# Performance work log

Measured on AMD Instinct MI355X. Metric: run time of the kernel, lower is better.

## Reference

```python
import jax, jax.numpy as jnp
import numpy as np

B, N, C, Q, H, RATIO = 8, 8700, 256, 300, 8, 4
D = C // H
HID = C * RATIO
EPS = 1e-5


def _ln(x, w, b):
    m = jnp.mean(x, axis=-1, keepdims=True)
    v = jnp.mean((x - m) ** 2, axis=-1, keepdims=True)
    return (x - m) * jax.lax.rsqrt(v + EPS) * w + b


def setup_inputs() -> dict:
    key = jax.random.key(0)
    ks = jax.random.split(key, 8)
    s = 0.02
    return {
        "x": jax.random.normal(ks[0], (B, N, C), jnp.float32),
        # linear weights stored [in, out] (y = x @ W), no biases (qkv_bias=False, Mlp bias=False)
        "Wq": jax.random.normal(ks[1], (C, C), jnp.float32) * s,
        "Wk": jax.random.normal(ks[2], (C, C), jnp.float32) * s,
        "Wv": jax.random.normal(ks[3], (C, C), jnp.float32) * s,
        "Wp": jax.random.normal(ks[4], (C, C), jnp.float32) * s,
        "W1": jax.random.normal(ks[5], (C, HID), jnp.float32) * s,
        "W2": jax.random.normal(ks[6], (HID, C), jnp.float32) * s,
        "ln1_w": jnp.ones((C,), jnp.float32),
        "ln1_b": jnp.zeros((C,), jnp.float32),
        "ln2_w": jnp.ones((C,), jnp.float32),
        "ln2_b": jnp.zeros((C,), jnp.float32),
        "gamma1": jnp.ones((C,), jnp.float32),
        "gamma2": jnp.ones((C,), jnp.float32),
    }


def reference(x, Wq, Wk, Wv, Wp, W1, W2, ln1_w, ln1_b, ln2_w, ln2_b, gamma1, gamma2):
    scale = D ** -0.5
    xn = _ln(x, ln1_w, ln1_b)                       # [B,N,C]
    # SAQAttn: queries only from the first Q tokens; keys/values from all N tokens
    q = (xn[:, :Q] @ Wq).reshape(B, Q, H, D) * scale  # [B,Q,H,D]
    k = (xn @ Wk).reshape(B, N, H, D)
    v = (xn @ Wv).reshape(B, N, H, D)
    attn = jax.nn.softmax(jnp.einsum('bqhd,bnhd->bhqn', q, k), axis=-1)  # [B,H,Q,N]
    x_det = jnp.einsum('bhqn,bnhd->bqhd', attn, v).reshape(B, Q, C) @ Wp  # [B,Q,C]
    # residual with layer-scale gamma1; context tokens pass normed features through
    x_attn = jnp.concatenate([x_det, xn[:, Q:]], axis=1)
    x = x + gamma1 * x_attn
    # tokens_norm=False: norm2 only on query tokens
    x = jnp.concatenate([_ln(x[:, :Q], ln2_w, ln2_b), x[:, Q:]], axis=1)
    # MLP on query tokens with layer-scale gamma2 (exact GELU, as nn.GELU default)
    det = gamma2 * (jax.nn.gelu(x[:, :Q] @ W1, approximate=False) @ W2)
    # faithful to source: x_res + cat([det, x[:,Q:]]) doubles the context tokens
    return x + jnp.concatenate([det, x[:, Q:]], axis=1)
```

## Files before the change

kernel.cpp:

```cpp
#include <hip/hip_runtime.h>

#define BB 8
#define NN 8700
#define CC 256
#define QQ 300
#define HH 8
#define DD 32
#define HIDN 1024
#define NSPLIT 12
#define TSTR (NSPLIT * 64)

typedef unsigned short u16;
typedef __attribute__((ext_vector_type(8))) short short8;
typedef __attribute__((ext_vector_type(4))) float f32x4;

#define MFMA16(a, b, c) __builtin_amdgcn_mfma_f32_16x16x32_bf16((a), (b), (c), 0, 0, 0)

__device__ __forceinline__ u16 f2bu(float f) {
    unsigned int u = __builtin_bit_cast(unsigned int, f);
    u += 0x7fffu + ((u >> 16) & 1u);
    return (u16)(u >> 16);
}
__device__ __forceinline__ unsigned int cvtpk(float lo, float hi) {
    unsigned int r;
    asm("v_cvt_pk_bf16_f32 %0, %1, %2" : "=v"(r) : "v"(lo), "v"(hi));
    return r;
}

__global__ __launch_bounds__(256)
void wprep_all(const float* __restrict__ Wq, const float* __restrict__ Wk,
               const float* __restrict__ Wv, const float* __restrict__ Wp,
               const float* __restrict__ W1, const float* __restrict__ W2,
               u16* __restrict__ dst, float qscale)
{
    int e = blockIdx.x * 256 + threadIdx.x;
    float v;
    if (e < 65536)       { int i = e;          int n = i >> 8, k = i & 255;   v = Wq[k * 256 + n] * qscale; }
    else if (e < 131072) { int i = e - 65536;  int n = i >> 8, k = i & 255;   v = Wk[k * 256 + n]; }
    else if (e < 196608) { int i = e - 131072; int n = i >> 8, k = i & 255;   v = Wv[k * 256 + n]; }
    else if (e < 262144) { int i = e - 196608; int n = i >> 8, k = i & 255;   v = Wp[k * 256 + n]; }
    else if (e < 524288) { int i = e - 262144; int n = i >> 8, k = i & 255;   v = W1[k * 1024 + n]; }
    else                 { int i = e - 524288; int n = i >> 10, k = i & 1023; v = W2[k * 256 + n]; }
    dst[e] = f2bu(v);
}

__global__ __launch_bounds__(256)
void ln1_k(const float* __restrict__ x, const float* __restrict__ w,
           const float* __restrict__ bv, const float* __restrict__ g1,
           u16* __restrict__ xn, float* __restrict__ out)
{
    int row = blockIdx.x * 4 + (threadIdx.x >> 6);
    int l = threadIdx.x & 63;
    size_t base = (size_t)row * CC + l * 4;
    float4 xv = *reinterpret_cast<const float4*>(x + base);
    float s  = xv.x + xv.y + xv.z + xv.w;
    float s2 = xv.x * xv.x + xv.y * xv.y + xv.z * xv.z + xv.w * xv.w;
#pragma unroll
    for (int m = 1; m < 64; m <<= 1) {
        s  += __shfl_xor(s,  m, 64);
        s2 += __shfl_xor(s2, m, 64);
    }
    float mean = s * (1.0f / CC);
    float rs = rsqrtf(s2 * (1.0f / CC) - mean * mean + 1e-5f);
    float4 wv = *reinterpret_cast<const float4*>(w  + l * 4);
    float4 bb = *reinterpret_cast<const float4*>(bv + l * 4);
    float n0 = (xv.x - mean) * rs * wv.x + bb.x;
    float n1 = (xv.y - mean) * rs * wv.y + bb.y;
    float n2 = (xv.z - mean) * rs * wv.z + bb.z;
    float n3 = (xv.w - mean) * rs * wv.w + bb.w;
    ushort4 u; u.x = f2bu(n0); u.y = f2bu(n1); u.z = f2bu(n2); u.w = f2bu(n3);
    *reinterpret_cast<ushort4*>(xn + base) = u;
    int n = row % NN;
    if (n >= QQ) {
        float4 gv = *reinterpret_cast<const float4*>(g1 + l * 4);
        float4 o;
        o.x = 2.0f * (xv.x + gv.x * n0);
        o.y = 2.0f * (xv.y + gv.y * n1);
        o.z = 2.0f * (xv.z + gv.z * n2);
        o.w = 2.0f * (xv.w + gv.w * n3);
        *reinterpret_cast<float4*>(out + base) = o;
    }
}

__global__ __launch_bounds__(256)
void ln2_k(const float* __restrict__ x, const float* __restrict__ pd,
           const float* __restrict__ g1, const float* __restrict__ w,
           const float* __restrict__ bv, float* __restrict__ xqf, u16* __restrict__ xqb)
{
    int r = blockIdx.x * 4 + (threadIdx.x >> 6);
    int l = threadIdx.x & 63;
    int b = r / QQ, n = r - b * QQ;
    size_t xoff = ((size_t)b * NN + n) * CC + l * 4;
    size_t roff = (size_t)r * CC + l * 4;
    float4 xv = *reinterpret_cast<const float4*>(x + xoff);
    float4 pv = *reinterpret_cast<const float4*>(pd + roff);
    float4 gv = *reinterpret_cast<const float4*>(g1 + l * 4);
    float x0 = xv.x + gv.x * pv.x;
    float x1 = xv.y + gv.y * pv.y;
    float x2 = xv.z + gv.z * pv.z;
    float x3 = xv.w + gv.w * pv.w;
    float s  = x0 + x1 + x2 + x3;
    float s2 = x0 * x0 + x1 * x1 + x2 * x2 + x3 * x3;
#pragma unroll
    for (int m = 1; m < 64; m <<= 1) {
        s  += __shfl_xor(s,  m, 64);
        s2 += __shfl_xor(s2, m, 64);
    }
    float mean = s * (1.0f / CC);
    float rs = rsqrtf(s2 * (1.0f / CC) - mean * mean + 1e-5f);
    float4 wv = *reinterpret_cast<const float4*>(w  + l * 4);
    float4 bb = *reinterpret_cast<const float4*>(bv + l * 4);
    float n0 = (x0 - mean) * rs * wv.x + bb.x;
    float n1 = (x1 - mean) * rs * wv.y + bb.y;
    float n2 = (x2 - mean) * rs * wv.z + bb.z;
    float n3 = (x3 - mean) * rs * wv.w + bb.w;
    float4 o; o.x = n0; o.y = n1; o.z = n2; o.w = n3;
    *reinterpret_cast<float4*>(xqf + roff) = o;
    ushort4 u; u.x = f2bu(n0); u.y = f2bu(n1); u.z = f2bu(n2); u.w = f2bu(n3);
    *reinterpret_cast<ushort4*>(xqb + roff) = u;
}

template<int EPI>
__global__ __launch_bounds__(256)
void gemm_k(const u16* __restrict__ A, const u16* __restrict__ WT,
            u16* __restrict__ Cb, u16* __restrict__ Cb2, float* __restrict__ Cf,
            const float* __restrict__ basep, const float* __restrict__ gvec,
            float* __restrict__ outp,
            int M, int K, int ldC, int rpb, int bstr)
{
    const int w = threadIdx.x >> 6, l = threadIdx.x & 63;
    const int l15 = l & 15, kg = l >> 4;
    const int rowbase = blockIdx.x * 64;
    const int colbase = blockIdx.y * 256 + w * 64;
    const short8 z8 = {0, 0, 0, 0, 0, 0, 0, 0};
    const f32x4 fz = {0.f, 0.f, 0.f, 0.f};

    const u16* ap[4]; bool av[4];
#pragma unroll
    for (int mi = 0; mi < 4; mi++) {
        int r = rowbase + mi * 16 + l15;
        av[mi] = (r < M);
        int rr = av[mi] ? r : 0;
        size_t ar = (size_t)(rr / rpb) * bstr + (rr % rpb);
        ap[mi] = A + ar * K + kg * 8;
    }
    const u16* bp[4];
#pragma unroll
    for (int ni = 0; ni < 4; ni++) {
        int col = colbase + ni * 16 + l15;
        bp[ni] = WT + (size_t)col * K + kg * 8;
    }
    f32x4 acc[4][4];
#pragma unroll
    for (int mi = 0; mi < 4; mi++)
#pragma unroll
        for (int ni = 0; ni < 4; ni++) acc[mi][ni] = fz;

    for (int ks = 0; ks < K; ks += 32) {
        short8 a[4], bfr[4];
#pragma unroll
        for (int mi = 0; mi < 4; mi++)
            a[mi] = av[mi] ? *reinterpret_cast<const short8*>(ap[mi] + ks) : z8;
#pragma unroll
        for (int ni = 0; ni < 4; ni++)
            bfr[ni] = *reinterpret_cast<const short8*>(bp[ni] + ks);
#pragma unroll
        for (int mi = 0; mi < 4; mi++)
#pragma unroll
            for (int ni = 0; ni < 4; ni++)
                acc[mi][ni] = MFMA16(a[mi], bfr[ni], acc[mi][ni]);
    }
#pragma unroll
    for (int mi = 0; mi < 4; mi++) {
#pragma unroll
        for (int j = 0; j < 4; j++) {
            int r = rowbase + mi * 16 + kg * 4 + j;
            if (r >= M) continue;
#pragma unroll
            for (int ni = 0; ni < 4; ni++) {
                int col = colbase + ni * 16 + l15;
                float v = acc[mi][ni][j];
                if (EPI == 0) {
                    if (col < CC) Cb[(size_t)r * ldC + col] = f2bu(v);
                    else          Cb2[(size_t)r * ldC + (col - CC)] = f2bu(v);
                } else if (EPI == 1) {
                    float gl = 0.5f * v * (1.0f + erff(v * 0.70710678118654752f));
                    Cb[(size_t)r * ldC + col] = f2bu(gl);
                } else if (EPI == 2) {
                    Cf[(size_t)r * ldC + col] = v;
                } else {
                    float res = basep[(size_t)r * CC + col] + gvec[col] * v;
                    size_t orow = (size_t)(r / QQ) * NN + (r % QQ);
                    outp[orow * CC + col] = res;
                }
            }
        }
    }
}

__global__ __launch_bounds__(256)
void attn_k(const u16* __restrict__ qm, const u16* __restrict__ km,
            const u16* __restrict__ vm, float* __restrict__ Op,
            float* __restrict__ lp)
{
    __shared__ u16 vt[2][32 * 64];
    __shared__ u16 plds[4][2][16 * 64];

    const int bx = blockIdx.x;
    const int split = bx >> 6;
    const int rem = bx & 63;
    const int h = rem >> 3, b = rem & 7;
    const int bh = b * HH + h;
    const int tid = threadIdx.x;
    const int w = tid >> 6, l = tid & 63;
    const int l15 = l & 15, kg = l >> 4;
    const int tstart = split * 64;
    const int nt = (NN - tstart + TSTR - 1) / TSTR;

    const f32x4 fz = {0.f, 0.f, 0.f, 0.f};

    const u16* kbase = km + (size_t)b * NN * CC + h * DD;
    const u16* vbase = vm + (size_t)b * NN * CC + h * DD;
    const int vkp = (tid & 31) * 2;
    const int vdg = (tid >> 5) * 4;

    short8 qfr[5];
#pragma unroll
    for (int qf = 0; qf < 5; qf++) {
        int qrow = w * 80 + qf * 16 + l15;
        int qc = qrow < QQ ? qrow : 0;
        qfr[qf] = *reinterpret_cast<const short8*>(qm + ((size_t)(b * QQ + qc) * CC + h * DD + kg * 8));
    }

    f32x4 o[2][5]; float lpart[5];
#pragma unroll
    for (int qf = 0; qf < 5; qf++) { o[0][qf] = fz; o[1][qf] = fz; lpart[qf] = 0.f; }

    short8 kf[4]; ushort4 v0r, v1r;
#pragma unroll
    for (int kb = 0; kb < 4; kb++) {
        int n = tstart + kb * 16 + l15; if (n > NN - 1) n = NN - 1;
        kf[kb] = *reinterpret_cast<const short8*>(kbase + (size_t)n * CC + kg * 8);
    }
    { int n0a = tstart + vkp;     if (n0a > NN - 1) n0a = NN - 1;
      int n0b = tstart + vkp + 1; if (n0b > NN - 1) n0b = NN - 1;
      v0r = *reinterpret_cast<const ushort4*>(vbase + (size_t)n0a * CC + vdg);
      v1r = *reinterpret_cast<const ushort4*>(vbase + (size_t)n0b * CC + vdg); }

    char* pl = (char*)plds[w];
    const int rdswz = ((l15 << 7) ^ ((l15 & 7) << 4)) + (kg << 4);
    const int wrbase = (l15 << 7) ^ ((l15 & 7) << 4);

    for (int t = 0; t < nt; ++t) {
        const int n0 = tstart + t * TSTR;
        char* vtb = (char*)vt[t & 1];
#pragma unroll
        for (int i = 0; i < 4; i++) {
            int row = vdg + i;
            unsigned int pk2 = (unsigned int)v0r[i] | ((unsigned int)v1r[i] << 16);
            int byteo = ((row << 7) + (vkp << 1)) ^ ((row & 7) << 4);
            *reinterpret_cast<unsigned int*>(vtb + byteo) = pk2;
        }
        __syncthreads();

        short8 kfn[4]; ushort4 v0n, v1n;
        { int n0n = (t + 1 < nt) ? n0 + TSTR : tstart;
#pragma unroll
          for (int kb = 0; kb < 4; kb++) {
              int n = n0n + kb * 16 + l15; if (n > NN - 1) n = NN - 1;
              kfn[kb] = *reinterpret_cast<const short8*>(kbase + (size_t)n * CC + kg * 8);
          }
          int na = n0n + vkp;     if (na > NN - 1) na = NN - 1;
          int nb = n0n + vkp + 1; if (nb > NN - 1) nb = NN - 1;
          v0n = *reinterpret_cast<const ushort4*>(vbase + (size_t)na * CC + vdg);
          v1n = *reinterpret_cast<const ushort4*>(vbase + (size_t)nb * CC + vdg); }

        short8 va[2][2];
#pragma unroll
        for (int ks = 0; ks < 2; ks++)
#pragma unroll
            for (int dg = 0; dg < 2; dg++) {
                int row = dg * 16 + l15;
                int byteo = ((row << 7) + 64 * ks + 16 * kg) ^ ((row & 7) << 4);
                va[ks][dg] = *reinterpret_cast<const short8*>(vtb + byteo);
            }

        const bool tail = (n0 + 64 > NN);

#pragma unroll
        for (int qf = 0; qf < 5; qf++) {
            short8 bp0, bp1;
            if (qf > 0) {
                const char* plr = pl + (((qf - 1) & 1) << 11);
                bp0 = *reinterpret_cast<const short8*>(plr + rdswz);
                bp1 = *reinterpret_cast<const short8*>(plr + rdswz + 64);
            }
            f32x4 s[4];
#pragma unroll
            for (int kb = 0; kb < 4; kb++)
                s[kb] = MFMA16(kf[kb], qfr[qf], fz);
            char* plw = pl + ((qf & 1) << 11);
            float ps = 0.f;
#pragma unroll
            for (int kb = 0; kb < 4; kb++) {
                float p0 = exp2f(s[kb][0]);
                float p1 = exp2f(s[kb][1]);
                float p2 = exp2f(s[kb][2]);
                float p3 = exp2f(s[kb][3]);
                if (tail) {
                    int kbase2 = n0 + 16 * kb + 4 * kg;
                    if (kbase2 + 0 >= NN) p0 = 0.f;
                    if (kbase2 + 1 >= NN) p1 = 0.f;
                    if (kbase2 + 2 >= NN) p2 = 0.f;
                    if (kbase2 + 3 >= NN) p3 = 0.f;
                }
                ps += (p0 + p1) + (p2 + p3);
                int byte0 = wrbase + ((16 * kb + 4 * kg) << 1);
                *reinterpret_cast<unsigned int*>(plw + byte0)     = cvtpk(p0, p1);
                *reinterpret_cast<unsigned int*>(plw + byte0 + 4) = cvtpk(p2, p3);
            }
            lpart[qf] += ps;
            if (qf > 0) {
                o[0][qf - 1] = MFMA16(va[0][0], bp0, o[0][qf - 1]);
                o[1][qf - 1] = MFMA16(va[0][1], bp0, o[1][qf - 1]);
                o[0][qf - 1] = MFMA16(va[1][0], bp1, o[0][qf - 1]);
                o[1][qf - 1] = MFMA16(va[1][1], bp1, o[1][qf - 1]);
            }
        }
        {
            const char* plr = pl + 0;
            short8 bp0 = *reinterpret_cast<const short8*>(plr + rdswz);
            short8 bp1 = *reinterpret_cast<const short8*>(plr + rdswz + 64);
            o[0][4] = MFMA16(va[0][0], bp0, o[0][4]);
            o[1][4] = MFMA16(va[0][1], bp0, o[1][4]);
            o[0][4] = MFMA16(va[1][0], bp1, o[0][4]);
            o[1][4] = MFMA16(va[1][1], bp1, o[1][4]);
        }
#pragma unroll
        for (int kb = 0; kb < 4; kb++) kf[kb] = kfn[kb];
        v0r = v0n; v1r = v1n;
    }

#pragma unroll
    for (int qf = 0; qf < 5; qf++) {
        lpart[qf] += __shfl_xor(lpart[qf], 16, 64);
        lpart[qf] += __shfl_xor(lpart[qf], 32, 64);
    }

    size_t pb = (size_t)(split * 64 + bh) * QQ;
#pragma unroll
    for (int qf = 0; qf < 5; qf++) {
        int q = w * 80 + qf * 16 + l15;
        if (q >= QQ) continue;
        size_t pr = pb + q;
        if (kg == 0) lp[pr] = lpart[qf];
        *reinterpret_cast<f32x4*>(Op + pr * DD + kg * 4)      = o[0][qf];
        *reinterpret_cast<f32x4*>(Op + pr * DD + 16 + kg * 4) = o[1][qf];
    }
}

__global__ __launch_bounds__(256)
void comb_k(const float* __restrict__ Op, const float* __restrict__ lp, u16* __restrict__ ao)
{
    int g = blockIdx.x * 256 + threadIdx.x;
    int d4 = (g & 7) * 4;
    int row = g >> 3;
    int bh = row / QQ, qq = row - bh * QQ;
    int b = bh >> 3, h = bh & 7;
    float L = 0.f, a0 = 0.f, a1 = 0.f, a2 = 0.f, a3 = 0.f;
#pragma unroll
    for (int s = 0; s < NSPLIT; s++) {
        size_t pr = (size_t)(s * 64 + bh) * QQ + qq;
        L += lp[pr];
        float4 ov = *reinterpret_cast<const float4*>(Op + pr * DD + d4);
        a0 += ov.x; a1 += ov.y; a2 += ov.z; a3 += ov.w;
    }
    float inv = 1.0f / L;
    ushort4 u;
    u.x = f2bu(a0 * inv); u.y = f2bu(a1 * inv); u.z = f2bu(a2 * inv); u.w = f2bu(a3 * inv);
    *reinterpret_cast<ushort4*>(ao + ((size_t)(b * QQ + qq) * CC + h * DD + d4)) = u;
}

extern "C" void kernel_launch(void* const* d_in, const int* in_sizes, int n_in,
                              void* d_out, int out_size, void* d_ws, size_t ws_size,
                              hipStream_t stream)
{
    (void)in_sizes; (void)n_in; (void)out_size; (void)ws_size;
    const float* x    = (const float*)d_in[0];
    const float* Wq   = (const float*)d_in[1];
    const float* Wk   = (const float*)d_in[2];
    const float* Wv   = (const float*)d_in[3];
    const float* Wp   = (const float*)d_in[4];
    const float* W1   = (const float*)d_in[5];
    const float* W2   = (const float*)d_in[6];
    const float* ln1w = (const float*)d_in[7];
    const float* ln1b = (const float*)d_in[8];
    const float* ln2w = (const float*)d_in[9];
    const float* ln2b = (const float*)d_in[10];
    const float* g1   = (const float*)d_in[11];
    const float* g2   = (const float*)d_in[12];
    float* out = (float*)d_out;

    char* p = (char*)d_ws;
    auto alloc = [&](size_t bytes) { char* r = p; p += (bytes + 255) & ~(size_t)255; return r; };

    const size_t MKV = (size_t)BB * NN;
    const size_t MQ  = (size_t)BB * QQ;

    u16* WqT  = (u16*)alloc((size_t)CC * CC * 2);
    u16* WkvT = (u16*)alloc((size_t)CC * CC * 2 * 2);
    u16* WpT  = (u16*)alloc((size_t)CC * CC * 2);
    u16* W1T  = (u16*)alloc((size_t)CC * HIDN * 2);
    u16* W2T  = (u16*)alloc((size_t)HIDN * CC * 2);
    u16* xn   = (u16*)alloc(MKV * CC * 2);
    u16* kbf  = (u16*)alloc(MKV * CC * 2);
    u16* vbf  = (u16*)alloc(MKV * CC * 2);
    u16* qbf  = (u16*)alloc(MQ * CC * 2);
    u16* aob  = (u16*)alloc(MQ * CC * 2);
    u16* xqb  = (u16*)alloc(MQ * CC * 2);
    u16* h1   = (u16*)alloc(MQ * HIDN * 2);
    float* pd  = (float*)alloc(MQ * CC * 4);
    float* xqf = (float*)alloc(MQ * CC * 4);
    float* Op  = (float*)alloc((size_t)NSPLIT * 64 * QQ * DD * 4);
    float* lp  = (float*)alloc((size_t)NSPLIT * 64 * QQ * 4);

    const float qscale = 0.17677669529663687f * 1.4426950408889634f;

    wprep_all<<<3072, 256, 0, stream>>>(Wq, Wk, Wv, Wp, W1, W2, WqT, qscale);

    ln1_k<<<(int)(MKV / 4), 256, 0, stream>>>(x, ln1w, ln1b, g1, xn, out);

    gemm_k<0><<<dim3(1088, 2), 256, 0, stream>>>(xn, WkvT, kbf, vbf, nullptr, nullptr, nullptr, nullptr,
                                                 (int)MKV, CC, CC, (int)MKV, 0);
    gemm_k<0><<<dim3(38, 1), 256, 0, stream>>>(xn, WqT, qbf, nullptr, nullptr, nullptr, nullptr, nullptr,
                                               (int)MQ, CC, CC, QQ, NN);

    attn_k<<<64 * NSPLIT, 256, 0, stream>>>(qbf, kbf, vbf, Op, lp);
    comb_k<<<(int)(MQ * 8 / 256), 256, 0, stream>>>(Op, lp, aob);

    gemm_k<2><<<dim3(38, 1), 256, 0, stream>>>(aob, WpT, nullptr, nullptr, pd, nullptr, nullptr, nullptr,
                                               (int)MQ, CC, CC, (int)MQ, 0);
    ln2_k<<<(int)(MQ / 4), 256, 0, stream>>>(x, pd, g1, ln2w, ln2b, xqf, xqb);

    gemm_k<1><<<dim3(38, 4), 256, 0, stream>>>(xqb, W1T, h1, nullptr, nullptr, nullptr, nullptr, nullptr,
                                               (int)MQ, CC, HIDN, (int)MQ, 0);
    gemm_k<3><<<dim3(38, 1), 256, 0, stream>>>(h1, W2T, nullptr, nullptr, nullptr, xqf, g2, out,
                                               (int)MQ, HIDN, CC, (int)MQ, 0);
}
```

Measured before the change: 268.9 us.

## Retune attention split and small GEMM tiles, compute row sums via MFMA

Raises the attention key-split count from 12 to 16 and drops the per-load bounds clamps by padding the K/V buffers with slack rows. The softmax row sum is now computed with an MFMA against a ones vector instead of scalar adds and shuffles. MFMA sections are wrapped in s_setprio. The small Q-side GEMMs switch to 16-row tiles so they launch more blocks. Together these aim to raise occupancy and cut VALU and branch work, at the cost of extra MFMA ops, more partial results to combine, and unclamped reads into the padding rows.

```diff
diff --git a/kernel.cpp b/kernel.cpp
--- a/kernel.cpp
+++ b/kernel.cpp
@@ -7,8 +7,9 @@
 #define HH 8
 #define DD 32
 #define HIDN 1024
-#define NSPLIT 12
+#define NSPLIT 16
 #define TSTR (NSPLIT * 64)
+#define KSLACK 1536
 
 typedef unsigned short u16;
 typedef __attribute__((ext_vector_type(8))) short short8;
@@ -120,7 +121,7 @@
     *reinterpret_cast<ushort4*>(xqb + roff) = u;
 }
 
-template<int EPI>
+template<int EPI, int MT>
 __global__ __launch_bounds__(256)
 void gemm_k(const u16* __restrict__ A, const u16* __restrict__ WT,
             u16* __restrict__ Cb, u16* __restrict__ Cb2, float* __restrict__ Cf,
@@ -128,16 +129,17 @@
             float* __restrict__ outp,
             int M, int K, int ldC, int rpb, int bstr)
 {
+    constexpr int NM = MT / 16;
     const int w = threadIdx.x >> 6, l = threadIdx.x & 63;
     const int l15 = l & 15, kg = l >> 4;
-    const int rowbase = blockIdx.x * 64;
+    const int rowbase = blockIdx.x * MT;
     const int colbase = blockIdx.y * 256 + w * 64;
     const short8 z8 = {0, 0, 0, 0, 0, 0, 0, 0};
     const f32x4 fz = {0.f, 0.f, 0.f, 0.f};
 
-    const u16* ap[4]; bool av[4];
-#pragma unroll
-    for (int mi = 0; mi < 4; mi++) {
+    const u16* ap[NM]; bool av[NM];
+#pragma unroll
+    for (int mi = 0; mi < NM; mi++) {
         int r = rowbase + mi * 16 + l15;
         av[mi] = (r < M);
         int rr = av[mi] ? r : 0;
@@ -150,28 +152,28 @@
         int col = colbase + ni * 16 + l15;
         bp[ni] = WT + (size_t)col * K + kg * 8;
     }
-    f32x4 acc[4][4];
-#pragma unroll
-    for (int mi = 0; mi < 4; mi++)
+    f32x4 acc[NM][4];
+#pragma unroll
+    for (int mi = 0; mi < NM; mi++)
 #pragma unroll
         for (int ni = 0; ni < 4; ni++) acc[mi][ni] = fz;
 
     for (int ks = 0; ks < K; ks += 32) {
-        short8 a[4], bfr[4];
-#pragma unroll
-        for (int mi = 0; mi < 4; mi++)
+        short8 a[NM], bfr[4];
+#pragma unroll
+        for (int mi = 0; mi < NM; mi++)
             a[mi] = av[mi] ? *reinterpret_cast<const short8*>(ap[mi] + ks) : z8;
 #pragma unroll
         for (int ni = 0; ni < 4; ni++)
             bfr[ni] = *reinterpret_cast<const short8*>(bp[ni] + ks);
 #pragma unroll
-        for (int mi = 0; mi < 4; mi++)
+        for (int mi = 0; mi < NM; mi++)
 #pragma unroll
             for (int ni = 0; ni < 4; ni++)
                 acc[mi][ni] = MFMA16(a[mi], bfr[ni], acc[mi][ni]);
     }
 #pragma unroll
-    for (int mi = 0; mi < 4; mi++) {
+    for (int mi = 0; mi < NM; mi++) {
 #pragma unroll
         for (int j = 0; j < 4; j++) {
             int r = rowbase + mi * 16 + kg * 4 + j;
@@ -218,6 +220,8 @@
     const int nt = (NN - tstart + TSTR - 1) / TSTR;
 
     const f32x4 fz = {0.f, 0.f, 0.f, 0.f};
+    const short os = (short)0x3F80;
+    const short8 ones = {os, os, os, os, os, os, os, os};
 
     const u16* kbase = km + (size_t)b * NN * CC + h * DD;
     const u16* vbase = vm + (size_t)b * NN * CC + h * DD;
@@ -238,14 +242,10 @@
 
     short8 kf[4]; ushort4 v0r, v1r;
 #pragma unroll
-    for (int kb = 0; kb < 4; kb++) {
-        int n = tstart + kb * 16 + l15; if (n > NN - 1) n = NN - 1;
-        kf[kb] = *reinterpret_cast<const short8*>(kbase + (size_t)n * CC + kg * 8);
-    }
-    { int n0a = tstart + vkp;     if (n0a > NN - 1) n0a = NN - 1;
-      int n0b = tstart + vkp + 1; if (n0b > NN - 1) n0b = NN - 1;
-      v0r = *reinterpret_cast<const ushort4*>(vbase + (size_t)n0a * CC + vdg);
-      v1r = *reinterpret_cast<const ushort4*>(vbase + (size_t)n0b * CC + vdg); }
+    for (int kb = 0; kb < 4; kb++)
+        kf[kb] = *reinterpret_cast<const short8*>(kbase + (size_t)(tstart + kb * 16 + l15) * CC + kg * 8);
+    v0r = *reinterpret_cast<const ushort4*>(vbase + (size_t)(tstart + vkp) * CC + vdg);
+    v1r = *reinterpret_cast<const ushort4*>(vbase + (size_t)(tstart + vkp + 1) * CC + vdg);
 
     char* pl = (char*)plds[w];
     const int rdswz = ((l15 << 7) ^ ((l15 & 7) << 4)) + (kg << 4);
@@ -264,16 +264,12 @@
         __syncthreads();
 
         short8 kfn[4]; ushort4 v0n, v1n;
-        { int n0n = (t + 1 < nt) ? n0 + TSTR : tstart;
-#pragma unroll
-          for (int kb = 0; kb < 4; kb++) {
-              int n = n0n + kb * 16 + l15; if (n > NN - 1) n = NN - 1;
-              kfn[kb] = *reinterpret_cast<const short8*>(kbase + (size_t)n * CC + kg * 8);
-          }
-          int na = n0n + vkp;     if (na > NN - 1) na = NN - 1;
-          int nb = n0n + vkp + 1; if (nb > NN - 1) nb = NN - 1;
-          v0n = *reinterpret_cast<const ushort4*>(vbase + (size_t)na * CC + vdg);
-          v1n = *reinterpret_cast<const ushort4*>(vbase + (size_t)nb * CC + vdg); }
+        { const int n0n = n0 + TSTR;
+#pragma unroll
+          for (int kb = 0; kb < 4; kb++)
+              kfn[kb] = *reinterpret_cast<const short8*>(kbase + (size_t)(n0n + kb * 16 + l15) * CC + kg * 8);
+          v0n = *reinterpret_cast<const ushort4*>(vbase + (size_t)(n0n + vkp) * CC + vdg);
+          v1n = *reinterpret_cast<const ushort4*>(vbase + (size_t)(n0n + vkp + 1) * CC + vdg); }
 
         short8 va[2][2];
 #pragma unroll
@@ -296,11 +292,12 @@
                 bp1 = *reinterpret_cast<const short8*>(plr + rdswz + 64);
             }
             f32x4 s[4];
+            __builtin_amdgcn_s_setprio(1);
 #pragma unroll
             for (int kb = 0; kb < 4; kb++)
                 s[kb] = MFMA16(kf[kb], qfr[qf], fz);
+            __builtin_amdgcn_s_setprio(0);
             char* plw = pl + ((qf & 1) << 11);
-            float ps = 0.f;
 #pragma unroll
             for (int kb = 0; kb < 4; kb++) {
                 float p0 = exp2f(s[kb][0]);
@@ -314,37 +311,39 @@
                     if (kbase2 + 2 >= NN) p2 = 0.f;
                     if (kbase2 + 3 >= NN) p3 = 0.f;
                 }
-                ps += (p0 + p1) + (p2 + p3);
                 int byte0 = wrbase + ((16 * kb + 4 * kg) << 1);
                 *reinterpret_cast<unsigned int*>(plw + byte0)     = cvtpk(p0, p1);
                 *reinterpret_cast<unsigned int*>(plw + byte0 + 4) = cvtpk(p2, p3);
             }
-            lpart[qf] += ps;
             if (qf > 0) {
+                __builtin_amdgcn_s_setprio(1);
                 o[0][qf - 1] = MFMA16(va[0][0], bp0, o[0][qf - 1]);
                 o[1][qf - 1] = MFMA16(va[0][1], bp0, o[1][qf - 1]);
                 o[0][qf - 1] = MFMA16(va[1][0], bp1, o[0][qf - 1]);
                 o[1][qf - 1] = MFMA16(va[1][1], bp1, o[1][qf - 1]);
+                f32x4 tsum = MFMA16(ones, bp0, fz);
+                tsum = MFMA16(ones, bp1, tsum);
+                __builtin_amdgcn_s_setprio(0);
+                lpart[qf - 1] += tsum[0];
             }
         }
         {
             const char* plr = pl + 0;
             short8 bp0 = *reinterpret_cast<const short8*>(plr + rdswz);
             short8 bp1 = *reinterpret_cast<const short8*>(plr + rdswz + 64);
+            __builtin_amdgcn_s_setprio(1);
             o[0][4] = MFMA16(va[0][0], bp0, o[0][4]);
             o[1][4] = MFMA16(va[0][1], bp0, o[1][4]);
             o[0][4] = MFMA16(va[1][0], bp1, o[0][4]);
             o[1][4] = MFMA16(va[1][1], bp1, o[1][4]);
+            f32x4 tsum = MFMA16(ones, bp0, fz);
+            tsum = MFMA16(ones, bp1, tsum);
+            __builtin_amdgcn_s_setprio(0);
+            lpart[4] += tsum[0];
         }
 #pragma unroll
         for (int kb = 0; kb < 4; kb++) kf[kb] = kfn[kb];
         v0r = v0n; v1r = v1n;
-    }
-
-#pragma unroll
-    for (int qf = 0; qf < 5; qf++) {
-        lpart[qf] += __shfl_xor(lpart[qf], 16, 64);
-        lpart[qf] += __shfl_xor(lpart[qf], 32, 64);
     }
 
     size_t pb = (size_t)(split * 64 + bh) * QQ;
@@ -413,8 +412,8 @@
     u16* W1T  = (u16*)alloc((size_t)CC * HIDN * 2);
     u16* W2T  = (u16*)alloc((size_t)HIDN * CC * 2);
     u16* xn   = (u16*)alloc(MKV * CC * 2);
-    u16* kbf  = (u16*)alloc(MKV * CC * 2);
-    u16* vbf  = (u16*)alloc(MKV * CC * 2);
+    u16* kbf  = (u16*)alloc((MKV + KSLACK) * CC * 2);
+    u16* vbf  = (u16*)alloc((MKV + KSLACK) * CC * 2);
     u16* qbf  = (u16*)alloc(MQ * CC * 2);
     u16* aob  = (u16*)alloc(MQ * CC * 2);
     u16* xqb  = (u16*)alloc(MQ * CC * 2);
@@ -430,20 +429,20 @@
 
     ln1_k<<<(int)(MKV / 4), 256, 0, stream>>>(x, ln1w, ln1b, g1, xn, out);
 
-    gemm_k<0><<<dim3(1088, 2), 256, 0, stream>>>(xn, WkvT, kbf, vbf, nullptr, nullptr, nullptr, nullptr,
-                                                 (int)MKV, CC, CC, (int)MKV, 0);
-    gemm_k<0><<<dim3(38, 1), 256, 0, stream>>>(xn, WqT, qbf, nullptr, nullptr, nullptr, nullptr, nullptr,
-                                               (int)MQ, CC, CC, QQ, NN);
+    gemm_k<0, 64><<<dim3(1088, 2), 256, 0, stream>>>(xn, WkvT, kbf, vbf, nullptr, nullptr, nullptr, nullptr,
+                                                     (int)MKV, CC, CC, (int)MKV, 0);
+    gemm_k<0, 16><<<dim3(150, 1), 256, 0, stream>>>(xn, WqT, qbf, nullptr, nullptr, nullptr, nullptr, nullptr,
+                                                    (int)MQ, CC, CC, QQ, NN);
 
     attn_k<<<64 * NSPLIT, 256, 0, stream>>>(qbf, kbf, vbf, Op, lp);
     comb_k<<<(int)(MQ * 8 / 256), 256, 0, stream>>>(Op, lp, aob);
 
-    gemm_k<2><<<dim3(38, 1), 256, 0, stream>>>(aob, WpT, nullptr, nullptr, pd, nullptr, nullptr, nullptr,
-                                               (int)MQ, CC, CC, (int)MQ, 0);
+    gemm_k<2, 16><<<dim3(150, 1), 256, 0, stream>>>(aob, WpT, nullptr, nullptr, pd, nullptr, nullptr, nullptr,
+                                                    (int)MQ, CC, CC, (int)MQ, 0);
     ln2_k<<<(int)(MQ / 4), 256, 0, stream>>>(x, pd, g1, ln2w, ln2b, xqf, xqb);
 
-    gemm_k<1><<<dim3(38, 4), 256, 0, stream>>>(xqb, W1T, h1, nullptr, nullptr, nullptr, nullptr, nullptr,
-                                               (int)MQ, CC, HIDN, (int)MQ, 0);
-    gemm_k<3><<<dim3(38, 1), 256, 0, stream>>>(h1, W2T, nullptr, nullptr, nullptr, xqf, g2, out,
-                                               (int)MQ, HIDN, CC, (int)MQ, 0);
-}
+    gemm_k<1, 16><<<dim3(150, 4), 256, 0, stream>>>(xqb, W1T, h1, nullptr, nullptr, nullptr, nullptr, nullptr,
+                                                    (int)MQ, CC, HIDN, (int)MQ, 0);
+    gemm_k<3, 16><<<dim3(150, 1), 256, 0, stream>>>(h1, W2T, nullptr, nullptr, nullptr, xqf, g2, out,
+                                                    (int)MQ, HIDN, CC, (int)MQ, 0);
+}
```

After: 247.7 us. -7.9%, faster.
